# Kernel tuning notes

Measured on AMD Instinct MI355X. Metric: run time of the kernel, lower is better.

The kernel has to match this reference:

```python
import jax, jax.numpy as jnp
import numpy as np
from functools import partial

B, R, C = 32, 300, 37            # frames, rois/frame, classes (incl. background)
SCORE_THR, NMS_THR = 0.1, 0.4    # thresholds from the source
BBOX_STD = jnp.array([0.1, 0.1, 0.2, 0.2], dtype=jnp.float32)
IMG_H, IMG_W, IMG_SCALE = 1067.0, 600.0, 1.6667


def setup_inputs() -> dict:
    key = jax.random.key(0)
    k1, k2, k3, k4, k5, k6 = jax.random.split(key, 6)
    # plausible RPN proposals inside the (scaled) image
    cx = jax.random.uniform(k1, (B, R)) * (IMG_W - 1.0)
    cy = jax.random.uniform(k2, (B, R)) * (IMG_H - 1.0)
    w = jax.random.uniform(k3, (B, R)) * 200.0 + 20.0
    h = jax.random.uniform(k4, (B, R)) * 200.0 + 20.0
    rois_boxes = jnp.stack([
        jnp.clip(cx - 0.5 * w, 0.0, IMG_W - 1.0),
        jnp.clip(cy - 0.5 * h, 0.0, IMG_H - 1.0),
        jnp.clip(cx + 0.5 * w, 0.0, IMG_W - 1.0),
        jnp.clip(cy + 0.5 * h, 0.0, IMG_H - 1.0)], axis=-1).astype(jnp.float32)
    bbox_pred = (jax.random.normal(k5, (B, R, 4 * C)) * 0.5).astype(jnp.float32)
    scores = jax.nn.softmax(jax.random.normal(k6, (B, R, C)) * 2.0, axis=-1).astype(jnp.float32)
    im_info = jnp.tile(jnp.array([IMG_H, IMG_W, IMG_SCALE], dtype=jnp.float32), (B, 1))
    return {"rois_boxes": rois_boxes, "bbox_pred": bbox_pred,
            "scores": scores, "im_info": im_info}


def _pairwise_iou(b):  # b: [R,4] -> [R,R], torchvision convention (no +1)
    area = (b[:, 2] - b[:, 0]) * (b[:, 3] - b[:, 1])
    lt = jnp.maximum(b[:, None, :2], b[None, :, :2])
    rb = jnp.minimum(b[:, None, 2:], b[None, :, 2:])
    wh = jnp.clip(rb - lt, 0.0)
    inter = wh[..., 0] * wh[..., 1]
    return inter / (area[:, None] + area[None, :] - inter + 1e-12)


def _nms_keep(boxes, scores):  # boxes [R,4], scores [R] -> bool keep mask [R]
    order = jnp.argsort(-scores)
    b, s = boxes[order], scores[order]
    iou = _pairwise_iou(b)                    # [R,R]
    idx = jnp.arange(R)
    valid = s > SCORE_THR

    def body(i, keep):
        sup = keep[i] & (iou[i] > NMS_THR) & (idx > i)
        return keep & ~sup

    keep_sorted = jax.lax.fori_loop(0, R, body, valid)
    return jnp.zeros(R, dtype=bool).at[order].set(keep_sorted)


def reference(rois_boxes, bbox_pred, scores, im_info):
    deltas = bbox_pred.reshape(B, R, C, 4) * BBOX_STD          # un-normalize
    x1, y1, x2, y2 = [rois_boxes[..., k] for k in range(4)]    # each [B,R]
    w = x2 - x1 + 1.0
    h = y2 - y1 + 1.0
    cx = x1 + 0.5 * w
    cy = y1 + 0.5 * h
    dx, dy, dw, dh = [deltas[..., k] for k in range(4)]        # each [B,R,C]
    pcx = dx * w[..., None] + cx[..., None]
    pcy = dy * h[..., None] + cy[..., None]
    pw = jnp.exp(dw) * w[..., None]
    ph = jnp.exp(dh) * h[..., None]
    px1 = pcx - 0.5 * pw
    py1 = pcy - 0.5 * ph
    px2 = pcx + 0.5 * pw
    py2 = pcy + 0.5 * ph
    # ---- clip_boxes to per-image (H, W) in scaled coords ----
    Wm1 = im_info[:, 1][:, None, None] - 1.0
    Hm1 = im_info[:, 0][:, None, None] - 1.0
    px1 = jnp.clip(px1, 0.0, Wm1)
    py1 = jnp.clip(py1, 0.0, Hm1)
    px2 = jnp.clip(px2, 0.0, Wm1)
    py2 = jnp.clip(py2, 0.0, Hm1)
    boxes = jnp.stack([px1, py1, px2, py2], axis=-1) / im_info[0, 2]  # [B,R,C,4]

    # ---- per-image, per-class NMS (classes 1..C-1, background skipped) ----
    cls_boxes = jnp.transpose(boxes[:, :, 1:, :], (0, 2, 1, 3))   # [B,C-1,R,4]
    cls_scores = jnp.transpose(scores[:, :, 1:], (0, 2, 1))       # [B,C-1,R]
    keep = jax.vmap(jax.vmap(_nms_keep))(cls_boxes, cls_scores)   # [B,C-1,R] bool

    # person class (j==1 -> slice index 0): keep only the single top detection
    sc0, k0 = cls_scores[:, 0, :], keep[:, 0, :]
    any0 = jnp.any(k0, axis=-1)
    top0 = jnp.argmax(jnp.where(k0, sc0, -jnp.inf), axis=-1)
    oh = (jnp.arange(R)[None, :] == top0[:, None]) & any0[:, None]
    keep = keep.at[:, 0, :].set(oh)

    # padded cls_dets: [B, C-1, R, 5], zeros where suppressed
    dets = jnp.concatenate([cls_boxes, cls_scores[..., None]], axis=-1)
    dets = jnp.clip(dets, 0.0) * keep[..., None].astype(dets.dtype)
    return dets
```

## Files before the change

### kernel.cpp

```cpp
#include <hip/hip_runtime.h>

#define RR 300
#define NCLS 37
#define COUT 36
#define NSTRIP 5
#define WPB 4
#define CAP2 128
#define SCORE_THR_C 0.1f
#define NMS_THR_C 0.4f

__device__ __forceinline__ float readlanef(float x, int sl) {
    return __uint_as_float((unsigned)__builtin_amdgcn_readlane((int)__float_as_uint(x), sl));
}

__global__ __launch_bounds__(256) void det_wave3_kernel(
    const float* __restrict__ rois,
    const float* __restrict__ pred,
    const float* __restrict__ scr,
    const float* __restrict__ iminfo,
    float* __restrict__ out)
{
#pragma clang fp contract(off)
    const int bid  = blockIdx.x;
    const int wid  = threadIdx.x >> 6;
    const int lane = threadIdx.x & 63;
    const int bc   = (bid & 7) * 144 + (bid >> 3) * WPB + wid;
    const int b    = bc / COUT;
    const int c    = bc % COUT;
    const int cls  = c + 1;

    __shared__ __align__(16) float csc[WPB][CAP2 + 4];
    __shared__ float4        cbx[WPB][CAP2];
    __shared__ int           cor[WPB][CAP2];
    __shared__ float4        sbx[WPB][CAP2];
    __shared__ int           sor[WPB][CAP2];
    __shared__ unsigned char kp[WPB][RR + 20];

    float4 ro[NSTRIP], pp[NSTRIP];
    float  ss[NSTRIP];
    #pragma unroll
    for (int t = 0; t < NSTRIP; ++t) {
        const int r = lane + 64 * t;
        kp[wid][r] = 0;
        if (r < RR) {
            ro[t] = *reinterpret_cast<const float4*>(rois + (size_t)(b * RR + r) * 4);
            pp[t] = *reinterpret_cast<const float4*>(pred + (size_t)(b * RR + r) * (4 * NCLS) + 4 * cls);
            ss[t] = scr[(size_t)(b * RR + r) * NCLS + cls];
        } else {
            ro[t] = make_float4(0.f, 0.f, 0.f, 0.f);
            pp[t] = make_float4(0.f, 0.f, 0.f, 0.f);
            ss[t] = 0.f;
        }
    }
    const float Hm1 = iminfo[b * 3 + 0] - 1.0f;
    const float Wm1 = iminfo[b * 3 + 1] - 1.0f;
    const float scl = iminfo[2];

    float4 bx[NSTRIP];
    bool   vv[NSTRIP];
    #pragma unroll
    for (int t = 0; t < NSTRIP; ++t) {
        const int r = lane + 64 * t;
        float w  = ro[t].z - ro[t].x + 1.0f;
        float h  = ro[t].w - ro[t].y + 1.0f;
        float cx = ro[t].x + 0.5f * w;
        float cy = ro[t].y + 0.5f * h;
        float dx = pp[t].x * 0.1f;
        float dy = pp[t].y * 0.1f;
        float dw = pp[t].z * 0.2f;
        float dh = pp[t].w * 0.2f;
        float pcx = dx * w + cx;
        float pcy = dy * h + cy;
        float pw  = expf(dw) * w;
        float ph  = expf(dh) * h;
        bx[t].x = fminf(fmaxf(pcx - 0.5f * pw, 0.0f), Wm1) / scl;
        bx[t].y = fminf(fmaxf(pcy - 0.5f * ph, 0.0f), Hm1) / scl;
        bx[t].z = fminf(fmaxf(pcx + 0.5f * pw, 0.0f), Wm1) / scl;
        bx[t].w = fminf(fmaxf(pcy + 0.5f * ph, 0.0f), Hm1) / scl;
        vv[t] = (r < RR) && (ss[t] > SCORE_THR_C);
    }

    const unsigned long long lmask = (1ull << lane) - 1ull;
    int pos[NSTRIP];
    int acc = 0;
    #pragma unroll
    for (int t = 0; t < NSTRIP; ++t) {
        const unsigned long long balt = __ballot(vv[t]);
        pos[t] = acc + __popcll(balt & lmask);
        acc   += __popcll(balt);
    }
    int nv = __builtin_amdgcn_readfirstlane(acc);
    if (nv > CAP2) nv = CAP2;

    #pragma unroll
    for (int t = 0; t < NSTRIP; ++t) {
        if (vv[t] && pos[t] < CAP2) {
            csc[wid][pos[t]] = ss[t];
            cbx[wid][pos[t]] = bx[t];
            cor[wid][pos[t]] = lane + 64 * t;
        }
    }
    if (lane < 4) csc[wid][nv + lane] = -1.0f;

    const bool has2 = (nv > 64);
    const bool a0 = (lane < nv);
    const bool a1 = has2 && (lane + 64 < nv);
    float  s0 = -2.f, s1 = -2.f;
    float4 b0 = make_float4(0.f, 0.f, 0.f, 0.f), b1 = b0;
    int    o0 = 0, o1 = 0;
    if (a0) { s0 = csc[wid][lane];      b0 = cbx[wid][lane];      o0 = cor[wid][lane]; }
    if (a1) { s1 = csc[wid][lane + 64]; b1 = cbx[wid][lane + 64]; o1 = cor[wid][lane + 64]; }

    int r0 = 0, r1 = 0;
    const float4* cs4 = reinterpret_cast<const float4*>(&csc[wid][0]);
    const int n4 = (nv + 3) >> 2;
    for (int q4 = 0; q4 < n4; ++q4) {
        const float4 sv = cs4[q4];
        const int qb = q4 * 4;
        r0 += (int)(sv.x > s0) + ((int)(sv.x == s0) & (int)(qb + 0 < lane));
        r0 += (int)(sv.y > s0) + ((int)(sv.y == s0) & (int)(qb + 1 < lane));
        r0 += (int)(sv.z > s0) + ((int)(sv.z == s0) & (int)(qb + 2 < lane));
        r0 += (int)(sv.w > s0) + ((int)(sv.w == s0) & (int)(qb + 3 < lane));
    }
    if (has2) {
        for (int q4 = 0; q4 < n4; ++q4) {
            const float4 sv = cs4[q4];
            const int qb = q4 * 4, me = lane + 64;
            r1 += (int)(sv.x > s1) + ((int)(sv.x == s1) & (int)(qb + 0 < me));
            r1 += (int)(sv.y > s1) + ((int)(sv.y == s1) & (int)(qb + 1 < me));
            r1 += (int)(sv.z > s1) + ((int)(sv.z == s1) & (int)(qb + 2 < me));
            r1 += (int)(sv.w > s1) + ((int)(sv.w == s1) & (int)(qb + 3 < me));
        }
    }

    if (a0) { sbx[wid][r0] = b0; sor[wid][r0] = o0; }
    if (a1) { sbx[wid][r1] = b1; sor[wid][r1] = o1; }
    float4 sb0 = make_float4(0.f, 0.f, 0.f, 0.f), sb1 = sb0;
    float  sa0 = 0.f, sa1 = 0.f;
    int    so0 = 0, so1 = 0;
    if (a0) { sb0 = sbx[wid][lane];      so0 = sor[wid][lane];
              sa0 = (sb0.z - sb0.x) * (sb0.w - sb0.y); }
    if (a1) { sb1 = sbx[wid][lane + 64]; so1 = sor[wid][lane + 64];
              sa1 = (sb1.z - sb1.x) * (sb1.w - sb1.y); }

    unsigned long long lv0, lv1, kb0 = 0ull, kb1 = 0ull;
    lv0 = (nv >= 64) ? ~0ull : ((1ull << nv) - 1ull);
    lv1 = has2 ? ((nv >= 128) ? ~0ull : ((1ull << (nv - 64)) - 1ull)) : 0ull;
    int top_orig = -1;
    for (;;) {
        int p;
        if (lv0)      p = __builtin_ctzll(lv0);
        else if (lv1) p = 64 + __builtin_ctzll(lv1);
        else          break;
        const int sp = __builtin_amdgcn_readfirstlane(p);

        float px1, py1, px2, py2;
        int   po;
        if (sp < 64) {
            px1 = readlanef(sb0.x, sp); py1 = readlanef(sb0.y, sp);
            px2 = readlanef(sb0.z, sp); py2 = readlanef(sb0.w, sp);
            po  = __builtin_amdgcn_readlane(so0, sp);
            kb0 |= 1ull << sp;  lv0 &= ~(1ull << sp);
        } else {
            const int sq = sp - 64;
            px1 = readlanef(sb1.x, sq); py1 = readlanef(sb1.y, sq);
            px2 = readlanef(sb1.z, sq); py2 = readlanef(sb1.w, sq);
            po  = __builtin_amdgcn_readlane(so1, sq);
            kb1 |= 1ull << sq;  lv1 &= ~(1ull << sq);
        }
        if (top_orig < 0) top_orig = po;
        const float pa = (px2 - px1) * (py2 - py1);

        {
            float lx = fmaxf(px1, sb0.x);
            float ly = fmaxf(py1, sb0.y);
            float rx = fminf(px2, sb0.z);
            float ry = fminf(py2, sb0.w);
            float iw = fmaxf(rx - lx, 0.0f);
            float ih = fmaxf(ry - ly, 0.0f);
            float inter = iw * ih;
            float den = pa + sa0 - inter + 1e-12f;
            float iou = inter / den;
            const unsigned long long m0 =
                __ballot(a0 && (lane > sp) && (iou > NMS_THR_C));
            lv0 &= ~m0;
        }
        if (has2) {
            float lx = fmaxf(px1, sb1.x);
            float ly = fmaxf(py1, sb1.y);
            float rx = fminf(px2, sb1.z);
            float ry = fminf(py2, sb1.w);
            float iw = fmaxf(rx - lx, 0.0f);
            float ih = fmaxf(ry - ly, 0.0f);
            float inter = iw * ih;
            float den = pa + sa1 - inter + 1e-12f;
            float iou = inter / den;
            const unsigned long long m1 =
                __ballot(a1 && (lane + 64 > sp) && (iou > NMS_THR_C));
            lv1 &= ~m1;
        }
    }

    if (a0 && ((kb0 >> lane) & 1ull)) kp[wid][so0] = 1;
    if (a1 && ((kb1 >> lane) & 1ull)) kp[wid][so1] = 1;

    #pragma unroll
    for (int t = 0; t < NSTRIP; ++t) {
        const int r = lane + 64 * t;
        if (r < RR) {
            const bool k = (c == 0) ? (r == top_orig) : (kp[wid][r] != 0);
            const float kf = k ? 1.0f : 0.0f;
            const size_t base = (((size_t)b * COUT + c) * RR + r) * 5;
            out[base + 0] = fmaxf(bx[t].x, 0.0f) * kf;
            out[base + 1] = fmaxf(bx[t].y, 0.0f) * kf;
            out[base + 2] = fmaxf(bx[t].z, 0.0f) * kf;
            out[base + 3] = fmaxf(bx[t].w, 0.0f) * kf;
            out[base + 4] = fmaxf(ss[t],  0.0f) * kf;
        }
    }
}

extern "C" void kernel_launch(void* const* d_in, const int* in_sizes, int n_in,
                              void* d_out, int out_size, void* d_ws, size_t ws_size,
                              hipStream_t stream) {
    const float* rois   = (const float*)d_in[0];
    const float* pred   = (const float*)d_in[1];
    const float* scores = (const float*)d_in[2];
    const float* iminfo = (const float*)d_in[3];
    float* out = (float*)d_out;
    det_wave3_kernel<<<dim3(288), dim3(256), 0, stream>>>(rois, pred, scores, iminfo, out);
}
```

Before: 19.20 us.

## Decode boxes only for valid candidates and launch one wave per block

Scores are loaded first and compacted, and only candidates above the score threshold fetch their roi and bbox-delta values and decode boxes. The decoded boxes of kept detections are written to shared memory for the output stage, so suppressed rows write zeros without any box math. The launch changes from 288 blocks of four waves to 1152 single-wave blocks, giving the scheduler finer-grained work and less shared memory per block. In exchange, the box loads become gathers that depend on the score loads, which adds a dependent-latency step.

```diff
diff --git a/kernel.cpp b/kernel.cpp
--- a/kernel.cpp
+++ b/kernel.cpp
@@ -4,7 +4,6 @@
 #define NCLS 37
 #define COUT 36
 #define NSTRIP 5
-#define WPB 4
 #define CAP2 128
 #define SCORE_THR_C 0.1f
 #define NMS_THR_C 0.4f
@@ -13,7 +12,7 @@
     return __uint_as_float((unsigned)__builtin_amdgcn_readlane((int)__float_as_uint(x), sl));
 }
 
-__global__ __launch_bounds__(256) void det_wave3_kernel(
+__global__ __launch_bounds__(64) void det_wave4_kernel(
     const float* __restrict__ rois,
     const float* __restrict__ pred,
     const float* __restrict__ scr,
@@ -22,97 +21,111 @@
 {
 #pragma clang fp contract(off)
     const int bid  = blockIdx.x;
-    const int wid  = threadIdx.x >> 6;
-    const int lane = threadIdx.x & 63;
-    const int bc   = (bid & 7) * 144 + (bid >> 3) * WPB + wid;
+    const int lane = threadIdx.x;
+    const int bc   = (bid & 7) * 144 + (bid >> 3);
     const int b    = bc / COUT;
     const int c    = bc % COUT;
     const int cls  = c + 1;
 
-    __shared__ __align__(16) float csc[WPB][CAP2 + 4];
-    __shared__ float4        cbx[WPB][CAP2];
-    __shared__ int           cor[WPB][CAP2];
-    __shared__ float4        sbx[WPB][CAP2];
-    __shared__ int           sor[WPB][CAP2];
-    __shared__ unsigned char kp[WPB][RR + 20];
-
-    float4 ro[NSTRIP], pp[NSTRIP];
-    float  ss[NSTRIP];
+    __shared__ __align__(16) float csc[CAP2 + 4];
+    __shared__ int          cro[CAP2];
+    __shared__ float4       sbx[CAP2];
+    __shared__ int          sor[CAP2];
+    __shared__ float4       vals4[RR];
+    __shared__ unsigned int kpz[80];
+
+    unsigned char* kp = (unsigned char*)kpz;
+    kpz[lane] = 0u;
+    if (lane < 16) kpz[64 + lane] = 0u;
+
+    float ss[NSTRIP];
+    bool  vv[NSTRIP];
     #pragma unroll
     for (int t = 0; t < NSTRIP; ++t) {
         const int r = lane + 64 * t;
-        kp[wid][r] = 0;
-        if (r < RR) {
-            ro[t] = *reinterpret_cast<const float4*>(rois + (size_t)(b * RR + r) * 4);
-            pp[t] = *reinterpret_cast<const float4*>(pred + (size_t)(b * RR + r) * (4 * NCLS) + 4 * cls);
-            ss[t] = scr[(size_t)(b * RR + r) * NCLS + cls];
-        } else {
-            ro[t] = make_float4(0.f, 0.f, 0.f, 0.f);
-            pp[t] = make_float4(0.f, 0.f, 0.f, 0.f);
-            ss[t] = 0.f;
-        }
-    }
+        ss[t] = (r < RR) ? scr[(size_t)(b * RR + r) * NCLS + cls] : 0.f;
+        vv[t] = (r < RR) && (ss[t] > SCORE_THR_C);
+    }
+
+    const unsigned long long lmask = (1ull << lane) - 1ull;
+    int pos[NSTRIP];
+    int acc = 0;
+    #pragma unroll
+    for (int t = 0; t < NSTRIP; ++t) {
+        const unsigned long long balt = __ballot(vv[t]);
+        pos[t] = acc + __popcll(balt & lmask);
+        acc   += __popcll(balt);
+    }
+    int nv = __builtin_amdgcn_readfirstlane(acc);
+    if (nv > CAP2) nv = CAP2;
+
+    #pragma unroll
+    for (int t = 0; t < NSTRIP; ++t) {
+        if (vv[t] && pos[t] < CAP2) {
+            csc[pos[t]] = ss[t];
+            cro[pos[t]] = lane + 64 * t;
+        }
+    }
+    if (lane < 4) csc[nv + lane] = -1.0f;
+
     const float Hm1 = iminfo[b * 3 + 0] - 1.0f;
     const float Wm1 = iminfo[b * 3 + 1] - 1.0f;
     const float scl = iminfo[2];
 
-    float4 bx[NSTRIP];
-    bool   vv[NSTRIP];
-    #pragma unroll
-    for (int t = 0; t < NSTRIP; ++t) {
-        const int r = lane + 64 * t;
-        float w  = ro[t].z - ro[t].x + 1.0f;
-        float h  = ro[t].w - ro[t].y + 1.0f;
-        float cx = ro[t].x + 0.5f * w;
-        float cy = ro[t].y + 0.5f * h;
-        float dx = pp[t].x * 0.1f;
-        float dy = pp[t].y * 0.1f;
-        float dw = pp[t].z * 0.2f;
-        float dh = pp[t].w * 0.2f;
+    const bool has2 = (nv > 64);
+    const bool a0 = (lane < nv);
+    const bool a1 = has2 && (lane + 64 < nv);
+
+    float  s0 = -2.f, s1 = -2.f;
+    int    o0 = 0, o1 = 0;
+    float4 b0 = make_float4(0.f, 0.f, 0.f, 0.f), b1 = b0;
+    if (a0) {
+        s0 = csc[lane];
+        o0 = cro[lane];
+        const float4 ro = *reinterpret_cast<const float4*>(rois + (size_t)(b * RR + o0) * 4);
+        const float4 pp = *reinterpret_cast<const float4*>(pred + (size_t)(b * RR + o0) * (4 * NCLS) + 4 * cls);
+        float w  = ro.z - ro.x + 1.0f;
+        float h  = ro.w - ro.y + 1.0f;
+        float cx = ro.x + 0.5f * w;
+        float cy = ro.y + 0.5f * h;
+        float dx = pp.x * 0.1f;
+        float dy = pp.y * 0.1f;
+        float dw = pp.z * 0.2f;
+        float dh = pp.w * 0.2f;
         float pcx = dx * w + cx;
         float pcy = dy * h + cy;
         float pw  = expf(dw) * w;
         float ph  = expf(dh) * h;
-        bx[t].x = fminf(fmaxf(pcx - 0.5f * pw, 0.0f), Wm1) / scl;
-        bx[t].y = fminf(fmaxf(pcy - 0.5f * ph, 0.0f), Hm1) / scl;
-        bx[t].z = fminf(fmaxf(pcx + 0.5f * pw, 0.0f), Wm1) / scl;
-        bx[t].w = fminf(fmaxf(pcy + 0.5f * ph, 0.0f), Hm1) / scl;
-        vv[t] = (r < RR) && (ss[t] > SCORE_THR_C);
-    }
-
-    const unsigned long long lmask = (1ull << lane) - 1ull;
-    int pos[NSTRIP];
-    int acc = 0;
-    #pragma unroll
-    for (int t = 0; t < NSTRIP; ++t) {
-        const unsigned long long balt = __ballot(vv[t]);
-        pos[t] = acc + __popcll(balt & lmask);
-        acc   += __popcll(balt);
-    }
-    int nv = __builtin_amdgcn_readfirstlane(acc);
-    if (nv > CAP2) nv = CAP2;
-
-    #pragma unroll
-    for (int t = 0; t < NSTRIP; ++t) {
-        if (vv[t] && pos[t] < CAP2) {
-            csc[wid][pos[t]] = ss[t];
-            cbx[wid][pos[t]] = bx[t];
-            cor[wid][pos[t]] = lane + 64 * t;
-        }
-    }
-    if (lane < 4) csc[wid][nv + lane] = -1.0f;
-
-    const bool has2 = (nv > 64);
-    const bool a0 = (lane < nv);
-    const bool a1 = has2 && (lane + 64 < nv);
-    float  s0 = -2.f, s1 = -2.f;
-    float4 b0 = make_float4(0.f, 0.f, 0.f, 0.f), b1 = b0;
-    int    o0 = 0, o1 = 0;
-    if (a0) { s0 = csc[wid][lane];      b0 = cbx[wid][lane];      o0 = cor[wid][lane]; }
-    if (a1) { s1 = csc[wid][lane + 64]; b1 = cbx[wid][lane + 64]; o1 = cor[wid][lane + 64]; }
+        b0.x = fminf(fmaxf(pcx - 0.5f * pw, 0.0f), Wm1) / scl;
+        b0.y = fminf(fmaxf(pcy - 0.5f * ph, 0.0f), Hm1) / scl;
+        b0.z = fminf(fmaxf(pcx + 0.5f * pw, 0.0f), Wm1) / scl;
+        b0.w = fminf(fmaxf(pcy + 0.5f * ph, 0.0f), Hm1) / scl;
+    }
+    if (a1) {
+        s1 = csc[lane + 64];
+        o1 = cro[lane + 64];
+        const float4 ro = *reinterpret_cast<const float4*>(rois + (size_t)(b * RR + o1) * 4);
+        const float4 pp = *reinterpret_cast<const float4*>(pred + (size_t)(b * RR + o1) * (4 * NCLS) + 4 * cls);
+        float w  = ro.z - ro.x + 1.0f;
+        float h  = ro.w - ro.y + 1.0f;
+        float cx = ro.x + 0.5f * w;
+        float cy = ro.y + 0.5f * h;
+        float dx = pp.x * 0.1f;
+        float dy = pp.y * 0.1f;
+        float dw = pp.z * 0.2f;
+        float dh = pp.w * 0.2f;
+        float pcx = dx * w + cx;
+        float pcy = dy * h + cy;
+        float pw  = expf(dw) * w;
+        float ph  = expf(dh) * h;
+        b1.x = fminf(fmaxf(pcx - 0.5f * pw, 0.0f), Wm1) / scl;
+        b1.y = fminf(fmaxf(pcy - 0.5f * ph, 0.0f), Hm1) / scl;
+        b1.z = fminf(fmaxf(pcx + 0.5f * pw, 0.0f), Wm1) / scl;
+        b1.w = fminf(fmaxf(pcy + 0.5f * ph, 0.0f), Hm1) / scl;
+    }
 
     int r0 = 0, r1 = 0;
-    const float4* cs4 = reinterpret_cast<const float4*>(&csc[wid][0]);
+    const float4* cs4 = reinterpret_cast<const float4*>(&csc[0]);
     const int n4 = (nv + 3) >> 2;
     for (int q4 = 0; q4 < n4; ++q4) {
         const float4 sv = cs4[q4];
@@ -133,14 +146,14 @@
         }
     }
 
-    if (a0) { sbx[wid][r0] = b0; sor[wid][r0] = o0; }
-    if (a1) { sbx[wid][r1] = b1; sor[wid][r1] = o1; }
+    if (a0) { sbx[r0] = b0; sor[r0] = o0; }
+    if (a1) { sbx[r1] = b1; sor[r1] = o1; }
     float4 sb0 = make_float4(0.f, 0.f, 0.f, 0.f), sb1 = sb0;
     float  sa0 = 0.f, sa1 = 0.f;
     int    so0 = 0, so1 = 0;
-    if (a0) { sb0 = sbx[wid][lane];      so0 = sor[wid][lane];
+    if (a0) { sb0 = sbx[lane];      so0 = sor[lane];
               sa0 = (sb0.z - sb0.x) * (sb0.w - sb0.y); }
-    if (a1) { sb1 = sbx[wid][lane + 64]; so1 = sor[wid][lane + 64];
+    if (a1) { sb1 = sbx[lane + 64]; so1 = sor[lane + 64];
               sa1 = (sb1.z - sb1.x) * (sb1.w - sb1.y); }
 
     unsigned long long lv0, lv1, kb0 = 0ull, kb1 = 0ull;
@@ -181,9 +194,7 @@
             float inter = iw * ih;
             float den = pa + sa0 - inter + 1e-12f;
             float iou = inter / den;
-            const unsigned long long m0 =
-                __ballot(a0 && (lane > sp) && (iou > NMS_THR_C));
-            lv0 &= ~m0;
+            lv0 &= ~__ballot(a0 && (lane > sp) && (iou > NMS_THR_C));
         }
         if (has2) {
             float lx = fmaxf(px1, sb1.x);
@@ -195,27 +206,33 @@
             float inter = iw * ih;
             float den = pa + sa1 - inter + 1e-12f;
             float iou = inter / den;
-            const unsigned long long m1 =
-                __ballot(a1 && (lane + 64 > sp) && (iou > NMS_THR_C));
-            lv1 &= ~m1;
-        }
-    }
-
-    if (a0 && ((kb0 >> lane) & 1ull)) kp[wid][so0] = 1;
-    if (a1 && ((kb1 >> lane) & 1ull)) kp[wid][so1] = 1;
+            lv1 &= ~__ballot(a1 && (lane + 64 > sp) && (iou > NMS_THR_C));
+        }
+    }
+
+    if (a0 && ((kb0 >> lane) & 1ull)) { vals4[so0] = sb0; kp[so0] = 1; }
+    if (a1 && ((kb1 >> lane) & 1ull)) { vals4[so1] = sb1; kp[so1] = 1; }
 
     #pragma unroll
     for (int t = 0; t < NSTRIP; ++t) {
         const int r = lane + 64 * t;
         if (r < RR) {
-            const bool k = (c == 0) ? (r == top_orig) : (kp[wid][r] != 0);
-            const float kf = k ? 1.0f : 0.0f;
+            const bool k = (c == 0) ? (r == top_orig) : (kp[r] != 0);
+            float q0 = 0.f, q1 = 0.f, q2 = 0.f, q3 = 0.f, q4 = 0.f;
+            if (k) {
+                const float4 v4 = vals4[r];
+                q0 = fmaxf(v4.x, 0.0f);
+                q1 = fmaxf(v4.y, 0.0f);
+                q2 = fmaxf(v4.z, 0.0f);
+                q3 = fmaxf(v4.w, 0.0f);
+                q4 = fmaxf(ss[t], 0.0f);
+            }
             const size_t base = (((size_t)b * COUT + c) * RR + r) * 5;
-            out[base + 0] = fmaxf(bx[t].x, 0.0f) * kf;
-            out[base + 1] = fmaxf(bx[t].y, 0.0f) * kf;
-            out[base + 2] = fmaxf(bx[t].z, 0.0f) * kf;
-            out[base + 3] = fmaxf(bx[t].w, 0.0f) * kf;
-            out[base + 4] = fmaxf(ss[t],  0.0f) * kf;
+            out[base + 0] = q0;
+            out[base + 1] = q1;
+            out[base + 2] = q2;
+            out[base + 3] = q3;
+            out[base + 4] = q4;
         }
     }
 }
@@ -228,5 +245,5 @@
     const float* scores = (const float*)d_in[2];
     const float* iminfo = (const float*)d_in[3];
     float* out = (float*)d_out;
-    det_wave3_kernel<<<dim3(288), dim3(256), 0, stream>>>(rois, pred, scores, iminfo, out);
+    det_wave4_kernel<<<dim3(1152), dim3(64), 0, stream>>>(rois, pred, scores, iminfo, out);
 }
```

After: 18.63 us, median of 2. 1.03x faster.
